# Optimization experiments

Measured on AMD Instinct MI355X. Metric: run time of the kernel, lower is better.

The kernel has to match this reference:

```python
import jax, jax.numpy as jnp
import numpy as np

RADIUS = 2                 # soft detection radius (init kwarg)
NMS_RADIUS = 2             # hardcoded in detect_keypoints: simple_nms(scores, 2)
TOP_K = 4096
TEMPERATURE = 0.1
KSIZE = 2 * RADIUS + 1     # 5
KK = KSIZE * KSIZE         # 25


def _hw_grid(dtype):
    # flatten order j = dy*KSIZE + dx ; entry = (x_off, y_off)  (torch's [:, [1,0]])
    lin = jnp.linspace(-RADIUS, RADIUS, KSIZE, dtype=dtype)
    gx, gy = jnp.meshgrid(lin, lin)  # 'xy': gx[dy,dx]=lin[dx], gy[dy,dx]=lin[dy]
    return jnp.stack([gx, gy], axis=-1).reshape(-1, 2)  # (KK, 2)


def _maxpool(x, r):
    k = 2 * r + 1
    return jax.lax.reduce_window(x, -jnp.inf, jax.lax.max,
                                 (1, 1, k, k), (1, 1, 1, 1),
                                 ((0, 0), (0, 0), (r, r), (r, r)))


def _simple_nms(scores, r):
    zeros = jnp.zeros_like(scores)
    max_mask = scores == _maxpool(scores, r)
    for _ in range(2):
        supp_mask = _maxpool(max_mask.astype(scores.dtype), r) > 0
        supp_scores = jnp.where(supp_mask, zeros, scores)
        new_max_mask = supp_scores == _maxpool(supp_scores, r)
        max_mask = max_mask | (new_max_mask & ~supp_mask)
    return jnp.where(max_mask, scores, zeros)


def _bilinear_zeros(img, xy):
    # img: (h, w); xy: (K, 2) normalized [-1,1]; align_corners=True, zero padding
    h, w = img.shape
    px = (xy[:, 0] + 1.0) * 0.5 * (w - 1)
    py = (xy[:, 1] + 1.0) * 0.5 * (h - 1)
    x0 = jnp.floor(px); y0 = jnp.floor(py)
    wx1 = px - x0; wx0 = 1.0 - wx1
    wy1 = py - y0; wy0 = 1.0 - wy1
    def tap(xi, yi, wgt):
        valid = (xi >= 0) & (xi < w) & (yi >= 0) & (yi < h)
        xc = jnp.clip(xi, 0, w - 1).astype(jnp.int32)
        yc = jnp.clip(yi, 0, h - 1).astype(jnp.int32)
        return jnp.where(valid, img[yc, xc], 0.0) * wgt
    return (tap(x0, y0, wx0 * wy0) + tap(x0 + 1, y0, wx1 * wy0)
            + tap(x0, y0 + 1, wx0 * wy1) + tap(x0 + 1, y0 + 1, wx1 * wy1))


def _dkd_forward(scores_map):
    b, c, h, w = scores_map.shape
    dtype = scores_map.dtype
    scores_nograd = jax.lax.stop_gradient(scores_map)

    nms_scores = _simple_nms(scores_nograd, NMS_RADIUS)
    # zero out border band of width RADIUS
    ybad = (jnp.arange(h) < RADIUS) | (jnp.arange(h) >= h - RADIUS)
    xbad = (jnp.arange(w) < RADIUS) | (jnp.arange(w) >= w - RADIUS)
    border = ybad[:, None] | xbad[None, :]
    nms_scores = jnp.where(border[None, None], 0.0, nms_scores)

    # top-k over flattened score map (per image)
    _, idx = jax.lax.top_k(nms_scores.reshape(b, -1), TOP_K)  # (b, K)
    ix = idx % w
    iy = idx // w

    # patch gather == unfold(scores_map) + gather, done sparsely with zero pad
    padded = jnp.pad(scores_map[:, 0], ((0, 0), (RADIUS, RADIUS), (RADIUS, RADIUS)))
    off = jnp.arange(KSIZE)
    ys = iy[:, :, None] + off[None, None, :]           # (b, K, KSIZE)
    xs = ix[:, :, None] + off[None, None, :]
    bidx = jnp.arange(b)[:, None, None, None]
    patch_scores = padded[bidx, ys[:, :, :, None], xs[:, :, None, :]]  # (b,K,KSIZE,KSIZE)
    patch_scores = patch_scores.reshape(b, TOP_K, KK)

    hw_grid = _hw_grid(dtype)                          # (KK, 2)
    max_v = jax.lax.stop_gradient(patch_scores.max(axis=-1, keepdims=True))
    x_exp = jnp.exp((patch_scores - max_v) / TEMPERATURE)   # (b,K,KK)
    x_exp_sum = x_exp.sum(axis=-1, keepdims=True)            # (b,K,1)
    xy_residual = jnp.einsum('bkp,pd->bkd', x_exp, hw_grid) / x_exp_sum  # (b,K,2)
    hw_dist2 = (((hw_grid[None, None] - xy_residual[:, :, None]) / RADIUS) ** 2).sum(-1)
    scoredispersity = (x_exp * hw_dist2).sum(-1) / x_exp_sum[..., 0]     # (b,K)

    keypoints_xy_nms = jnp.stack([ix, iy], axis=-1).astype(dtype)
    wh = jnp.array([w - 1, h - 1], dtype=dtype)
    keypoints_xy = (keypoints_xy_nms + xy_residual) / wh * 2.0 - 1.0     # (b,K,2)

    kptscore = jax.vmap(_bilinear_zeros)(scores_map[:, 0], keypoints_xy)  # (b,K)
    return keypoints_xy, kptscore, scoredispersity


def setup_inputs() -> dict:
    key = jax.random.key(0)
    scores_map = jax.random.uniform(key, (8, 1, 1024, 1024), dtype=jnp.float32)
    return {"scores_map": scores_map}


def reference(scores_map):
    # matches torch forward: (keypoints, kptscores, scoredispersitys)
    return _dkd_forward(scores_map)
```

## Files before the change

kernel.cpp:

```cpp
#include <hip/hip_runtime.h>
#include <stdint.h>

namespace {

constexpr int B = 8;
constexpr int H = 1024;
constexpr int W = 1024;
constexpr int TOPK = 4096;
constexpr int CAND_CAP = 131072;
constexpr int SEL_CAP = 16384;
constexpr int LIST_CAP = 320;
constexpr int HIST_N = 32768;
constexpr int NCHUNK = 32;
constexpr int NHB = 48;

constexpr int RROWS = 92;
constexpr int NG = 22;
constexpr int STR = 88;
constexpr int MW4 = 4;
constexpr int NSTRIP = 11;
constexpr int NUNIT = NG * NSTRIP;

constexpr int RK_ME = 256;
constexpr int RK_CH = 1024;

constexpr size_t OFF_CNT   = 0;
constexpr size_t OFF_GHIST = 4096;
constexpr size_t OFF_RANK  = OFF_GHIST + (size_t)B * HIST_N * 4;
constexpr size_t OFF_SEL   = OFF_RANK + (size_t)B * SEL_CAP * 4;
constexpr size_t OFF_TOPK  = OFF_SEL + (size_t)B * SEL_CAP * 8;
constexpr size_t OFF_CAND  = OFF_TOPK + (size_t)B * TOPK * 8;
constexpr size_t MEMSET_BYTES = OFF_RANK + (size_t)B * SEL_CAP * 4;

__device__ __forceinline__ float max5(float a, float b, float c, float d, float e) {
  return fmaxf(fmaxf(fmaxf(a, b), fmaxf(c, d)), e);
}
__device__ __forceinline__ float4 ld4(const float* p) {
  return *reinterpret_cast<const float4*>(p);
}

template <int PASS>
__device__ __forceinline__ void score_pass(
    int u, int x0, int y0, const float* __restrict__ S,
    const uint32_t* __restrict__ SUP, uint32_t* __restrict__ MA,
    uint64_t* list, uint32_t* cnt_loc, uint64_t* cand, uint32_t* cand_count, int b) {
  const int G = u % NG, s = u / NG;
  const int r0 = 2 + 8 * s;
  const int gx0 = x0 - 12 + 4 * G;
  uint32_t colm = 0;
#pragma unroll
  for (int j = 0; j < 4; ++j)
    if ((unsigned)(gx0 + j) < (unsigned)W) colm |= 1u << j;
  const int p = 4 * G - 4;
  const int pw = (p < 0) ? 0 : (p >> 5);
  const int psh = (p < 0) ? 0 : (p & 31);
  const int pls = (p < 0) ? -p : 0;

  float4 hw[5], cw[5];
  uint32_t sn[5];
#pragma unroll
  for (int k = 0; k < 12; ++k) {
    const int rr = r0 - 2 + k;
    const float* rowp = S + rr * STR + 4 * G;
    float4 d = ld4(rowp);
    float4 a = (G > 0) ? ld4(rowp - 4) : d;
    float4 e = (G < NG - 1) ? ld4(rowp + 4) : d;
    uint32_t supn = 0;
    if (PASS != 0) {
      const uint32_t* srow = SUP + rr * MW4;
      uint64_t X = (uint64_t)srow[pw] | ((uint64_t)srow[pw + 1] << 32);
      uint64_t win = pls ? (X << pls) : (X >> psh);
      if (win & 0x001u) a.x = 0.f;
      if (win & 0x002u) a.y = 0.f;
      if (win & 0x004u) a.z = 0.f;
      if (win & 0x008u) a.w = 0.f;
      if (win & 0x010u) d.x = 0.f;
      if (win & 0x020u) d.y = 0.f;
      if (win & 0x040u) d.z = 0.f;
      if (win & 0x080u) d.w = 0.f;
      if (win & 0x100u) e.x = 0.f;
      if (win & 0x200u) e.y = 0.f;
      if (win & 0x400u) e.z = 0.f;
      if (win & 0x800u) e.w = 0.f;
      supn = (uint32_t)(win >> 4) & 0xFu;
    }
    float4 hm;
    hm.x = max5(a.z, a.w, d.x, d.y, d.z);
    hm.y = max5(a.w, d.x, d.y, d.z, d.w);
    hm.z = max5(d.x, d.y, d.z, d.w, e.x);
    hm.w = max5(d.y, d.z, d.w, e.x, e.y);
    hw[k % 5] = hm;
    cw[k % 5] = d;
    sn[k % 5] = supn;
    if (k >= 4) {
      const int rq = r0 + k - 4;
      const int gy = y0 - 12 + rq;
      float4 vm;
      vm.x = max5(hw[0].x, hw[1].x, hw[2].x, hw[3].x, hw[4].x);
      vm.y = max5(hw[0].y, hw[1].y, hw[2].y, hw[3].y, hw[4].y);
      vm.z = max5(hw[0].z, hw[1].z, hw[2].z, hw[3].z, hw[4].z);
      vm.w = max5(hw[0].w, hw[1].w, hw[2].w, hw[3].w, hw[4].w);
      float4 c = cw[(k + 3) % 5];
      uint32_t nm = (uint32_t)(c.x == vm.x) | ((uint32_t)(c.y == vm.y) << 1) |
                    ((uint32_t)(c.z == vm.z) << 2) | ((uint32_t)(c.w == vm.w) << 3);
      nm &= ((unsigned)gy < (unsigned)H) ? colm : 0u;
      const int widx = rq * MW4 + (G >> 3);
      const int shift = 4 * (G & 7);
      if (PASS == 0) {
        if (nm) atomicOr(&MA[widx], nm << shift);
      } else if (PASS == 1) {
        uint32_t v = nm & ~sn[(k + 3) % 5];
        if (v) atomicOr(&MA[widx], v << shift);
      } else {
        uint32_t fin = ((MA[widx] >> shift) & 0xFu) | (nm & ~sn[(k + 3) % 5]);
        if (fin && G >= 3 && G < 19 && rq >= 12 && rq < 76 && gy >= 2 && gy < H - 2) {
#pragma unroll
          for (int j = 0; j < 4; ++j) {
            if ((fin >> j) & 1u) {
              int gx = gx0 + j;
              if (gx >= 2 && gx < W - 2) {
                float sval = S[rq * STR + 4 * G + j];
                if (sval > 0.0f) {
                  uint32_t bits = __float_as_uint(sval);
                  uint32_t flat = (uint32_t)(gy * W + gx);
                  uint64_t key = ((uint64_t)bits << 32) | (uint64_t)(0xFFFFFFFFu - flat);
                  uint32_t pos = atomicAdd(cnt_loc, 1u);
                  if (pos < (uint32_t)LIST_CAP) {
                    list[pos] = key;
                  } else {
                    uint32_t pp = atomicAdd(&cand_count[b], 1u);
                    if (pp < (uint32_t)CAND_CAP) cand[(size_t)b * CAND_CAP + pp] = key;
                  }
                }
              }
            }
          }
        }
      }
    }
  }
}

__device__ __forceinline__ void dilate_pass(int u, int x0, int y0,
                                            const uint32_t* __restrict__ MIN_,
                                            uint32_t* __restrict__ SOUT) {
  const int G = u % NG, s = u / NG;
  const int r0 = 2 + 8 * s;
  const int gx0 = x0 - 12 + 4 * G;
  uint32_t colm = 0;
#pragma unroll
  for (int j = 0; j < 4; ++j)
    if ((unsigned)(gx0 + j) < (unsigned)W) colm |= 1u << j;
  const int p = 4 * G - 2;
  const int pw = (p < 0) ? 0 : (p >> 5);
  const int psh = (p < 0) ? 0 : (p & 31);
  const int pls = (p < 0) ? -p : 0;
  uint32_t ring[5];
#pragma unroll
  for (int k = 0; k < 12; ++k) {
    const int rr = r0 - 2 + k;
    const uint32_t* srow = MIN_ + rr * MW4;
    uint64_t X = (uint64_t)srow[pw] | ((uint64_t)srow[pw + 1] << 32);
    uint64_t win = pls ? (X << pls) : (X >> psh);
    uint64_t t = win | (win >> 1) | (win >> 2) | (win >> 3) | (win >> 4);
    ring[k % 5] = (uint32_t)t & 0xFu;
    if (k >= 4) {
      const int rq = r0 + k - 4;
      const int gy = y0 - 12 + rq;
      uint32_t nib = ring[0] | ring[1] | ring[2] | ring[3] | ring[4];
      nib &= ((unsigned)gy < (unsigned)H) ? colm : 0u;
      if (nib) atomicOr(&SOUT[rq * MW4 + (G >> 3)], nib << (4 * (G & 7)));
    }
  }
}

__global__ void __launch_bounds__(256, 4) k_nms(const float* __restrict__ scores,
                                                uint64_t* __restrict__ cand,
                                                uint32_t* __restrict__ cand_count) {
  __shared__ float S[RROWS * STR];
  __shared__ uint32_t MAs[RROWS * MW4];
  __shared__ uint32_t SP1[RROWS * MW4];
  __shared__ uint32_t SP2[RROWS * MW4];
  __shared__ uint64_t list[LIST_CAP];
  __shared__ uint32_t cnt_loc, base_g;
  const int b = blockIdx.z;
  const int x0 = blockIdx.x * 64, y0 = blockIdx.y * 64;
  const int tid = threadIdx.x;
  const float* img = scores + (size_t)b * H * W;
  if (tid == 0) cnt_loc = 0;

  for (int u = tid; u < RROWS * NG; u += 256) {
    int r = u / NG, G = u % NG;
    int gy = y0 - 12 + r, gx = x0 - 12 + 4 * G;
    float4 v;
    if ((unsigned)gy < (unsigned)H && (unsigned)gx < (unsigned)W)
      v = ld4(img + (size_t)gy * W + gx);
    else
      v = make_float4(-INFINITY, -INFINITY, -INFINITY, -INFINITY);
    *reinterpret_cast<float4*>(&S[r * STR + 4 * G]) = v;
  }
  for (int i = tid; i < RROWS * MW4; i += 256) {
    MAs[i] = 0;
    SP1[i] = 0;
    SP2[i] = 0;
  }
  __syncthreads();
  if (tid < NUNIT)
    score_pass<0>(tid, x0, y0, S, nullptr, MAs, nullptr, nullptr, nullptr, nullptr, b);
  __syncthreads();
  if (tid < NUNIT) dilate_pass(tid, x0, y0, MAs, SP1);
  __syncthreads();
  if (tid < NUNIT)
    score_pass<1>(tid, x0, y0, S, SP1, MAs, nullptr, nullptr, nullptr, nullptr, b);
  __syncthreads();
  if (tid < NUNIT) dilate_pass(tid, x0, y0, MAs, SP2);
  __syncthreads();
  if (tid < NUNIT)
    score_pass<2>(tid, x0, y0, S, SP2, MAs, list, &cnt_loc, cand, cand_count, b);
  __syncthreads();
  uint32_t nblk = cnt_loc;
  uint32_t nmain = nblk < (uint32_t)LIST_CAP ? nblk : (uint32_t)LIST_CAP;
  if (tid == 0) base_g = atomicAdd(&cand_count[b], nmain);
  __syncthreads();
  uint32_t bg = base_g;
  for (uint32_t i = tid; i < nmain; i += 256) {
    uint32_t pp = bg + i;
    if (pp < (uint32_t)CAND_CAP) cand[(size_t)b * CAND_CAP + pp] = list[i];
  }
}

__global__ void __launch_bounds__(256) k_hist(const uint64_t* __restrict__ cand,
                                              const uint32_t* __restrict__ cand_count,
                                              uint32_t* __restrict__ ghist) {
  const int b = blockIdx.y;
  uint32_t n = cand_count[b];
  if (n > (uint32_t)CAND_CAP) n = CAND_CAP;
  uint32_t* gh = ghist + (size_t)b * HIST_N;
  const uint64_t* cb = cand + (size_t)b * CAND_CAP;
  const int lane = threadIdx.x & 63;
  for (uint32_t i = blockIdx.x * 256 + threadIdx.x;; i += NHB * 256) {
    bool valid = i < n;
    uint64_t act = __ballot(valid);
    if (!act) break;
    uint32_t bkt = 0;
    if (valid) bkt = (uint32_t)(cb[i] >> 47);
    uint64_t peers = act;
#pragma unroll
    for (int bit = 0; bit < 15; ++bit) {
      uint64_t bb = __ballot((bkt >> bit) & 1u);
      peers &= ((bkt >> bit) & 1u) ? bb : ~bb;
    }
    if (valid && (__ffsll((unsigned long long)peers) - 1) == lane)
      atomicAdd(&gh[bkt], (uint32_t)__popcll((unsigned long long)peers));
  }
}

__global__ void __launch_bounds__(256) k_chunksum(const uint32_t* __restrict__ ghist,
                                                  uint32_t* __restrict__ gchunk) {
  const int b = blockIdx.y, c = blockIdx.x;
  const uint32_t* gh = ghist + (size_t)b * HIST_N + c * 1024;
  uint32_t s = 0;
#pragma unroll
  for (int j = 0; j < 4; ++j) s += gh[threadIdx.x + 256 * j];
#pragma unroll
  for (int m = 1; m < 64; m <<= 1) s += __shfl_xor(s, m);
  __shared__ uint32_t red[4];
  if ((threadIdx.x & 63) == 0) red[threadIdx.x >> 6] = s;
  __syncthreads();
  if (threadIdx.x == 0) gchunk[b * NCHUNK + c] = red[0] + red[1] + red[2] + red[3];
}

__global__ void __launch_bounds__(1024) k_findthr(const uint32_t* __restrict__ ghist,
                                                  const uint32_t* __restrict__ gchunk,
                                                  uint64_t* __restrict__ thr_key) {
  __shared__ uint32_t ch[NCHUNK];
  __shared__ uint32_t h[1024];
  __shared__ int shCC;
  __shared__ uint32_t sh_above;
  const int b = blockIdx.x, t = threadIdx.x;
  if (t < NCHUNK) ch[t] = gchunk[b * NCHUNK + t];
  __syncthreads();
  if (t == 0) {
    uint32_t run = 0;
    int CC = -1;
    uint32_t above = 0;
    for (int c = NCHUNK - 1; c >= 0; --c) {
      uint32_t nrun = run + ch[c];
      if (run < (uint32_t)TOPK && nrun >= (uint32_t)TOPK) { CC = c; above = run; }
      run = nrun;
    }
    if (run < (uint32_t)TOPK) CC = -1;
    shCC = CC;
    sh_above = above;
  }
  __syncthreads();
  const int CC = shCC;
  if (CC < 0) {
    if (t == 0) thr_key[b] = 0ull;
    return;
  }
  const uint32_t above = sh_above;
  h[t] = ghist[(size_t)b * HIST_N + CC * 1024 + t];
  __syncthreads();
  for (int d = 1; d < 1024; d <<= 1) {
    uint32_t v = (t + d < 1024) ? h[t + d] : 0u;
    __syncthreads();
    h[t] += v;
    __syncthreads();
  }
  uint32_t cum = above + h[t];
  uint32_t cumn = (t + 1 < 1024) ? above + h[t + 1] : above;
  if (cum >= (uint32_t)TOPK && cumn < (uint32_t)TOPK)
    thr_key[b] = (uint64_t)(CC * 1024 + t) << 47;
}

__global__ void __launch_bounds__(1024) k_compact(const uint64_t* __restrict__ cand,
                                                  const uint32_t* __restrict__ cand_count,
                                                  const uint64_t* __restrict__ thr_key,
                                                  uint64_t* __restrict__ sel,
                                                  uint32_t* __restrict__ sel_count) {
  __shared__ uint64_t list[1024];
  __shared__ uint32_t cnt_loc;
  __shared__ uint32_t base_g;
  const int b = blockIdx.y;
  uint32_t n = cand_count[b];
  if (n > (uint32_t)CAND_CAP) n = CAND_CAP;
  const int tid = threadIdx.x;
  if (tid == 0) cnt_loc = 0;
  __syncthreads();
  uint32_t i = blockIdx.x * 1024 + tid;
  if (i < n) {
    uint64_t key = cand[(size_t)b * CAND_CAP + i];
    if (key >= thr_key[b]) {
      uint32_t pos = atomicAdd(&cnt_loc, 1u);
      list[pos] = key;
    }
  }
  __syncthreads();
  uint32_t nblk = cnt_loc;
  if (tid == 0 && nblk > 0) base_g = atomicAdd(&sel_count[b], nblk);
  __syncthreads();
  if (nblk > 0 && (uint32_t)tid < nblk) {
    uint32_t pp = base_g + tid;
    if (pp < (uint32_t)SEL_CAP) sel[(size_t)b * SEL_CAP + pp] = list[tid];
  }
}

__global__ void __launch_bounds__(RK_ME) k_rank_part(const uint64_t* __restrict__ sel,
                                                     const uint32_t* __restrict__ sel_count,
                                                     uint32_t* __restrict__ rankg) {
  __shared__ uint64_t keys[RK_CH];
  const int b = blockIdx.z;
  uint32_t n = sel_count[b];
  if (n > (uint32_t)SEL_CAP) n = SEL_CAP;
  const uint32_t me0 = blockIdx.x * RK_ME;
  const uint32_t c0 = blockIdx.y * RK_CH;
  if (me0 >= n || c0 >= n) return;
  const uint64_t* sb = sel + (size_t)b * SEL_CAP;
  uint32_t clen = n - c0;
  if (clen > (uint32_t)RK_CH) clen = RK_CH;
  for (uint32_t i = threadIdx.x; i < clen; i += RK_ME) keys[i] = sb[c0 + i];
  __syncthreads();
  const uint32_t me = me0 + threadIdx.x;
  if (me >= n) return;
  const uint64_t kme = sb[me];
  uint32_t rank = 0;
  uint32_t i = 0;
  for (; i + 8 <= clen; i += 8) {
    rank += (keys[i] > kme);
    rank += (keys[i + 1] > kme);
    rank += (keys[i + 2] > kme);
    rank += (keys[i + 3] > kme);
    rank += (keys[i + 4] > kme);
    rank += (keys[i + 5] > kme);
    rank += (keys[i + 6] > kme);
    rank += (keys[i + 7] > kme);
  }
  for (; i < clen; ++i) rank += (keys[i] > kme);
  if (rank) atomicAdd(&rankg[(size_t)b * SEL_CAP + me], rank);
}

__global__ void __launch_bounds__(256) k_scatter(const uint64_t* __restrict__ sel,
                                                 const uint32_t* __restrict__ sel_count,
                                                 const uint32_t* __restrict__ rankg,
                                                 uint64_t* __restrict__ topk) {
  const int b = blockIdx.y;
  uint32_t n = sel_count[b];
  if (n > (uint32_t)SEL_CAP) n = SEL_CAP;
  uint32_t i = blockIdx.x * 256 + threadIdx.x;
  if (i >= n) return;
  uint32_t r = rankg[(size_t)b * SEL_CAP + i];
  if (r < (uint32_t)TOPK) topk[(size_t)b * TOPK + r] = sel[(size_t)b * SEL_CAP + i];
}

__global__ void __launch_bounds__(256) k_refine(const float* __restrict__ scores,
                                                const uint64_t* __restrict__ topk,
                                                float* __restrict__ out) {
  int gid = blockIdx.x * 256 + threadIdx.x;
  int kp = gid >> 3, ln = gid & 7;
  const int b = kp / TOPK;
  const int k = kp % TOPK;
  uint64_t key = topk[(size_t)b * TOPK + k];
  uint32_t flat = 0xFFFFFFFFu - (uint32_t)(key & 0xFFFFFFFFull);
  if (flat >= (uint32_t)(H * W)) flat = 0;
  const int ix = (int)(flat % W);
  const int iy = (int)(flat / W);
  const float* img = scores + (size_t)b * H * W;

  const int nt = (ln == 0) ? 4 : 3;
  float v[4];
  float mymax = -INFINITY;
#pragma unroll
  for (int i = 0; i < 4; ++i) {
    if (i < nt) {
      int t = ln + 8 * i;
      int y = iy + t / 5 - 2, x = ix + t % 5 - 2;
      float val = ((unsigned)x < (unsigned)W && (unsigned)y < (unsigned)H)
                      ? img[(size_t)y * W + x] : 0.0f;
      v[i] = val;
      mymax = fmaxf(mymax, val);
    }
  }
#pragma unroll
  for (int m = 1; m < 8; m <<= 1) mymax = fmaxf(mymax, __shfl_xor(mymax, m));
  float e[4];
  float sum = 0.f, sx = 0.f, sy = 0.f;
#pragma unroll
  for (int i = 0; i < 4; ++i) {
    if (i < nt) {
      int t = ln + 8 * i;
      float ev = expf((v[i] - mymax) / 0.1f);
      e[i] = ev;
      sum += ev;
      sx += ev * (float)(t % 5 - 2);
      sy += ev * (float)(t / 5 - 2);
    }
  }
#pragma unroll
  for (int m = 1; m < 8; m <<= 1) {
    sum += __shfl_xor(sum, m);
    sx += __shfl_xor(sx, m);
    sy += __shfl_xor(sy, m);
  }
  float rx = sx / sum, ry = sy / sum;
  float dsp = 0.f;
#pragma unroll
  for (int i = 0; i < 4; ++i) {
    if (i < nt) {
      int t = ln + 8 * i;
      float dx = ((float)(t % 5 - 2) - rx) * 0.5f;
      float dy = ((float)(t / 5 - 2) - ry) * 0.5f;
      dsp += e[i] * (dx * dx + dy * dy);
    }
  }
#pragma unroll
  for (int m = 1; m < 8; m <<= 1) dsp += __shfl_xor(dsp, m);
  if (ln != 0) return;
  dsp /= sum;
  float kx = ((float)ix + rx) / 1023.0f * 2.0f - 1.0f;
  float ky = ((float)iy + ry) / 1023.0f * 2.0f - 1.0f;
  float px = (kx + 1.0f) * 0.5f * 1023.0f;
  float py = (ky + 1.0f) * 0.5f * 1023.0f;
  float x0f = floorf(px), y0f = floorf(py);
  float wx1 = px - x0f, wx0 = 1.0f - wx1;
  float wy1 = py - y0f, wy0 = 1.0f - wy1;
  int x0 = (int)x0f, y0 = (int)y0f;
  float sc = 0.0f;
  {
    int xs[2] = {x0, x0 + 1};
    int ys[2] = {y0, y0 + 1};
    float wxs[2] = {wx0, wx1};
    float wys[2] = {wy0, wy1};
#pragma unroll
    for (int yy = 0; yy < 2; ++yy)
#pragma unroll
      for (int xx = 0; xx < 2; ++xx) {
        int xi = xs[xx], yi = ys[yy];
        bool valid = (xi >= 0 && xi < W && yi >= 0 && yi < H);
        int xc = min(max(xi, 0), W - 1);
        int yc = min(max(yi, 0), H - 1);
        float vv = valid ? img[(size_t)yc * W + xc] : 0.0f;
        sc += vv * (wxs[xx] * wys[yy]);
      }
  }
  out[((size_t)b * TOPK + k) * 2 + 0] = kx;
  out[((size_t)b * TOPK + k) * 2 + 1] = ky;
  out[(size_t)B * TOPK * 2 + (size_t)b * TOPK + k] = sc;
  out[(size_t)B * TOPK * 3 + (size_t)b * TOPK + k] = dsp;
}

}

extern "C" void kernel_launch(void* const* d_in, const int* in_sizes, int n_in,
                              void* d_out, int out_size, void* d_ws, size_t ws_size,
                              hipStream_t stream) {
  const float* scores = (const float*)d_in[0];
  float* out = (float*)d_out;
  char* ws = (char*)d_ws;

  uint32_t* cnt = (uint32_t*)(ws + OFF_CNT);
  uint32_t* cand_count = cnt;
  uint32_t* sel_count  = cnt + 8;
  uint64_t* thr_key    = (uint64_t*)(cnt + 16);
  uint32_t* gchunk     = cnt + 256;
  uint32_t* ghist = (uint32_t*)(ws + OFF_GHIST);
  uint32_t* rankg = (uint32_t*)(ws + OFF_RANK);
  uint64_t* sel  = (uint64_t*)(ws + OFF_SEL);
  uint64_t* topk = (uint64_t*)(ws + OFF_TOPK);
  uint64_t* cand = (uint64_t*)(ws + OFF_CAND);

  hipMemsetAsync(ws + OFF_CNT, 0, MEMSET_BYTES, stream);

  k_nms<<<dim3(W / 64, H / 64, B), 256, 0, stream>>>(scores, cand, cand_count);
  k_hist<<<dim3(NHB, B), 256, 0, stream>>>(cand, cand_count, ghist);
  k_chunksum<<<dim3(NCHUNK, B), 256, 0, stream>>>(ghist, gchunk);
  k_findthr<<<B, 1024, 0, stream>>>(ghist, gchunk, thr_key);
  k_compact<<<dim3(CAND_CAP / 1024, B), 1024, 0, stream>>>(cand, cand_count, thr_key, sel, sel_count);
  k_rank_part<<<dim3(SEL_CAP / RK_ME, SEL_CAP / RK_CH, B), RK_ME, 0, stream>>>(sel, sel_count, rankg);
  k_scatter<<<dim3(SEL_CAP / 256, B), 256, 0, stream>>>(sel, sel_count, rankg, topk);
  k_refine<<<(B * TOPK * 8) / 256, 256, 0, stream>>>(scores, topk, out);
}
```

Baseline: 224.9 us.

## Fuse rank, scatter and refine kernels; merge chunk-sum into threshold search

The rank-partial, scatter and refine kernels become one kernel. Each block ranks its slice of selected keys against all selected keys in shared-memory chunks, then refines the keypoints and writes them straight to their rank position. Chunk summation is folded into the threshold kernel, which now builds a 1024-way coarse prefix scan followed by a serial fine search. The memset is replaced with a zeroing kernel, and the selection capacity is halved. These changes remove several launches and the global rank and topk buffers, but each rank block now loops over every key serially, and a halved SEL_CAP could overflow if ties at the threshold bucket are large.

Result: slower. 269.1 us (+19.6%).

```diff
diff --git a/kernel.cpp b/kernel.cpp
--- a/kernel.cpp
+++ b/kernel.cpp
@@ -8,10 +8,9 @@
 constexpr int W = 1024;
 constexpr int TOPK = 4096;
 constexpr int CAND_CAP = 131072;
-constexpr int SEL_CAP = 16384;
+constexpr int SEL_CAP = 8192;
 constexpr int LIST_CAP = 320;
 constexpr int HIST_N = 32768;
-constexpr int NCHUNK = 32;
 constexpr int NHB = 48;
 
 constexpr int RROWS = 92;
@@ -21,16 +20,13 @@
 constexpr int NSTRIP = 11;
 constexpr int NUNIT = NG * NSTRIP;
 
-constexpr int RK_ME = 256;
 constexpr int RK_CH = 1024;
 
 constexpr size_t OFF_CNT   = 0;
 constexpr size_t OFF_GHIST = 4096;
-constexpr size_t OFF_RANK  = OFF_GHIST + (size_t)B * HIST_N * 4;
-constexpr size_t OFF_SEL   = OFF_RANK + (size_t)B * SEL_CAP * 4;
-constexpr size_t OFF_TOPK  = OFF_SEL + (size_t)B * SEL_CAP * 8;
-constexpr size_t OFF_CAND  = OFF_TOPK + (size_t)B * TOPK * 8;
-constexpr size_t MEMSET_BYTES = OFF_RANK + (size_t)B * SEL_CAP * 4;
+constexpr size_t OFF_SEL   = OFF_GHIST + (size_t)B * HIST_N * 4;
+constexpr size_t OFF_CAND  = OFF_SEL + (size_t)B * SEL_CAP * 8;
+constexpr size_t ZERO_BYTES = OFF_SEL;
 
 __device__ __forceinline__ float max5(float a, float b, float c, float d, float e) {
   return fmaxf(fmaxf(fmaxf(a, b), fmaxf(c, d)), e);
@@ -229,6 +225,13 @@
   }
 }
 
+__global__ void __launch_bounds__(256) k_zero(float4* __restrict__ p, int n4) {
+  int i = blockIdx.x * 256 + threadIdx.x;
+  const int stride = gridDim.x * 256;
+  const float4 z = make_float4(0.f, 0.f, 0.f, 0.f);
+  for (; i < n4; i += stride) p[i] = z;
+}
+
 __global__ void __launch_bounds__(256) k_hist(const uint64_t* __restrict__ cand,
                                               const uint32_t* __restrict__ cand_count,
                                               uint32_t* __restrict__ ghist) {
@@ -255,63 +258,45 @@
   }
 }
 
-__global__ void __launch_bounds__(256) k_chunksum(const uint32_t* __restrict__ ghist,
-                                                  uint32_t* __restrict__ gchunk) {
-  const int b = blockIdx.y, c = blockIdx.x;
-  const uint32_t* gh = ghist + (size_t)b * HIST_N + c * 1024;
-  uint32_t s = 0;
-#pragma unroll
-  for (int j = 0; j < 4; ++j) s += gh[threadIdx.x + 256 * j];
-#pragma unroll
-  for (int m = 1; m < 64; m <<= 1) s += __shfl_xor(s, m);
-  __shared__ uint32_t red[4];
-  if ((threadIdx.x & 63) == 0) red[threadIdx.x >> 6] = s;
-  __syncthreads();
-  if (threadIdx.x == 0) gchunk[b * NCHUNK + c] = red[0] + red[1] + red[2] + red[3];
-}
-
 __global__ void __launch_bounds__(1024) k_findthr(const uint32_t* __restrict__ ghist,
-                                                  const uint32_t* __restrict__ gchunk,
                                                   uint64_t* __restrict__ thr_key) {
-  __shared__ uint32_t ch[NCHUNK];
-  __shared__ uint32_t h[1024];
-  __shared__ int shCC;
+  __shared__ uint32_t part[1024];
+  __shared__ int shT;
   __shared__ uint32_t sh_above;
   const int b = blockIdx.x, t = threadIdx.x;
-  if (t < NCHUNK) ch[t] = gchunk[b * NCHUNK + t];
-  __syncthreads();
-  if (t == 0) {
-    uint32_t run = 0;
-    int CC = -1;
-    uint32_t above = 0;
-    for (int c = NCHUNK - 1; c >= 0; --c) {
-      uint32_t nrun = run + ch[c];
-      if (run < (uint32_t)TOPK && nrun >= (uint32_t)TOPK) { CC = c; above = run; }
-      run = nrun;
-    }
-    if (run < (uint32_t)TOPK) CC = -1;
-    shCC = CC;
-    sh_above = above;
-  }
-  __syncthreads();
-  const int CC = shCC;
-  if (CC < 0) {
+  const uint32_t* gh = ghist + (size_t)b * HIST_N;
+  uint32_t s = 0;
+#pragma unroll 4
+  for (int i = 0; i < 32; ++i) s += gh[t * 32 + i];
+  part[t] = s;
+  if (t == 0) { shT = -1; sh_above = 0; }
+  __syncthreads();
+  for (int d = 1; d < 1024; d <<= 1) {
+    uint32_t v = (t + d < 1024) ? part[t + d] : 0u;
+    __syncthreads();
+    part[t] += v;
+    __syncthreads();
+  }
+  if (part[0] < (uint32_t)TOPK) {
     if (t == 0) thr_key[b] = 0ull;
     return;
   }
-  const uint32_t above = sh_above;
-  h[t] = ghist[(size_t)b * HIST_N + CC * 1024 + t];
-  __syncthreads();
-  for (int d = 1; d < 1024; d <<= 1) {
-    uint32_t v = (t + d < 1024) ? h[t + d] : 0u;
-    __syncthreads();
-    h[t] += v;
-    __syncthreads();
-  }
-  uint32_t cum = above + h[t];
-  uint32_t cumn = (t + 1 < 1024) ? above + h[t + 1] : above;
-  if (cum >= (uint32_t)TOPK && cumn < (uint32_t)TOPK)
-    thr_key[b] = (uint64_t)(CC * 1024 + t) << 47;
+  {
+    uint32_t mine = part[t];
+    uint32_t nxt = (t + 1 < 1024) ? part[t + 1] : 0u;
+    if (mine >= (uint32_t)TOPK && nxt < (uint32_t)TOPK) { shT = t; sh_above = nxt; }
+  }
+  __syncthreads();
+  if (t == 0) {
+    const int T = shT;
+    uint32_t run = sh_above;
+    int bkt = T * 32;
+    for (int i = 31; i >= 0; --i) {
+      run += gh[T * 32 + i];
+      if (run >= (uint32_t)TOPK) { bkt = T * 32 + i; break; }
+    }
+    thr_key[b] = (uint64_t)bkt << 47;
+  }
 }
 
 __global__ void __launch_bounds__(1024) k_compact(const uint64_t* __restrict__ cand,
@@ -346,147 +331,139 @@
   }
 }
 
-__global__ void __launch_bounds__(RK_ME) k_rank_part(const uint64_t* __restrict__ sel,
-                                                     const uint32_t* __restrict__ sel_count,
-                                                     uint32_t* __restrict__ rankg) {
+__global__ void __launch_bounds__(256) k_rankref(const float* __restrict__ scores,
+                                                 const uint64_t* __restrict__ sel,
+                                                 const uint32_t* __restrict__ sel_count,
+                                                 float* __restrict__ out) {
   __shared__ uint64_t keys[RK_CH];
-  const int b = blockIdx.z;
-  uint32_t n = sel_count[b];
-  if (n > (uint32_t)SEL_CAP) n = SEL_CAP;
-  const uint32_t me0 = blockIdx.x * RK_ME;
-  const uint32_t c0 = blockIdx.y * RK_CH;
-  if (me0 >= n || c0 >= n) return;
-  const uint64_t* sb = sel + (size_t)b * SEL_CAP;
-  uint32_t clen = n - c0;
-  if (clen > (uint32_t)RK_CH) clen = RK_CH;
-  for (uint32_t i = threadIdx.x; i < clen; i += RK_ME) keys[i] = sb[c0 + i];
-  __syncthreads();
-  const uint32_t me = me0 + threadIdx.x;
-  if (me >= n) return;
-  const uint64_t kme = sb[me];
-  uint32_t rank = 0;
-  uint32_t i = 0;
-  for (; i + 8 <= clen; i += 8) {
-    rank += (keys[i] > kme);
-    rank += (keys[i + 1] > kme);
-    rank += (keys[i + 2] > kme);
-    rank += (keys[i + 3] > kme);
-    rank += (keys[i + 4] > kme);
-    rank += (keys[i + 5] > kme);
-    rank += (keys[i + 6] > kme);
-    rank += (keys[i + 7] > kme);
-  }
-  for (; i < clen; ++i) rank += (keys[i] > kme);
-  if (rank) atomicAdd(&rankg[(size_t)b * SEL_CAP + me], rank);
-}
-
-__global__ void __launch_bounds__(256) k_scatter(const uint64_t* __restrict__ sel,
-                                                 const uint32_t* __restrict__ sel_count,
-                                                 const uint32_t* __restrict__ rankg,
-                                                 uint64_t* __restrict__ topk) {
+  __shared__ uint64_t kks[256];
+  __shared__ uint32_t rks[256];
   const int b = blockIdx.y;
   uint32_t n = sel_count[b];
   if (n > (uint32_t)SEL_CAP) n = SEL_CAP;
-  uint32_t i = blockIdx.x * 256 + threadIdx.x;
-  if (i >= n) return;
-  uint32_t r = rankg[(size_t)b * SEL_CAP + i];
-  if (r < (uint32_t)TOPK) topk[(size_t)b * TOPK + r] = sel[(size_t)b * SEL_CAP + i];
-}
-
-__global__ void __launch_bounds__(256) k_refine(const float* __restrict__ scores,
-                                                const uint64_t* __restrict__ topk,
-                                                float* __restrict__ out) {
-  int gid = blockIdx.x * 256 + threadIdx.x;
-  int kp = gid >> 3, ln = gid & 7;
-  const int b = kp / TOPK;
-  const int k = kp % TOPK;
-  uint64_t key = topk[(size_t)b * TOPK + k];
-  uint32_t flat = 0xFFFFFFFFu - (uint32_t)(key & 0xFFFFFFFFull);
-  if (flat >= (uint32_t)(H * W)) flat = 0;
-  const int ix = (int)(flat % W);
-  const int iy = (int)(flat / W);
+  const uint32_t me0 = blockIdx.x * 256;
+  if (me0 >= n) return;
+  const uint64_t* sb = sel + (size_t)b * SEL_CAP;
+  const int tid = threadIdx.x;
+  const uint32_t me = me0 + tid;
+  const uint64_t kme = (me < n) ? sb[me] : 0ull;
+  uint32_t rank = 0;
+  for (uint32_t c0 = 0; c0 < n; c0 += RK_CH) {
+    uint32_t clen = n - c0;
+    if (clen > (uint32_t)RK_CH) clen = RK_CH;
+    __syncthreads();
+    for (uint32_t i = tid; i < clen; i += 256) keys[i] = sb[c0 + i];
+    __syncthreads();
+    uint32_t i = 0;
+    for (; i + 8 <= clen; i += 8) {
+      rank += (keys[i] > kme);
+      rank += (keys[i + 1] > kme);
+      rank += (keys[i + 2] > kme);
+      rank += (keys[i + 3] > kme);
+      rank += (keys[i + 4] > kme);
+      rank += (keys[i + 5] > kme);
+      rank += (keys[i + 6] > kme);
+      rank += (keys[i + 7] > kme);
+    }
+    for (; i < clen; ++i) rank += (keys[i] > kme);
+  }
+  rks[tid] = (me < n && rank < (uint32_t)TOPK) ? rank : 0xFFFFFFFFu;
+  kks[tid] = kme;
+  __syncthreads();
+
   const float* img = scores + (size_t)b * H * W;
-
-  const int nt = (ln == 0) ? 4 : 3;
-  float v[4];
-  float mymax = -INFINITY;
-#pragma unroll
-  for (int i = 0; i < 4; ++i) {
-    if (i < nt) {
-      int t = ln + 8 * i;
-      int y = iy + t / 5 - 2, x = ix + t % 5 - 2;
-      float val = ((unsigned)x < (unsigned)W && (unsigned)y < (unsigned)H)
-                      ? img[(size_t)y * W + x] : 0.0f;
-      v[i] = val;
-      mymax = fmaxf(mymax, val);
-    }
-  }
-#pragma unroll
-  for (int m = 1; m < 8; m <<= 1) mymax = fmaxf(mymax, __shfl_xor(mymax, m));
-  float e[4];
-  float sum = 0.f, sx = 0.f, sy = 0.f;
-#pragma unroll
-  for (int i = 0; i < 4; ++i) {
-    if (i < nt) {
-      int t = ln + 8 * i;
-      float ev = expf((v[i] - mymax) / 0.1f);
-      e[i] = ev;
-      sum += ev;
-      sx += ev * (float)(t % 5 - 2);
-      sy += ev * (float)(t / 5 - 2);
-    }
-  }
-#pragma unroll
-  for (int m = 1; m < 8; m <<= 1) {
-    sum += __shfl_xor(sum, m);
-    sx += __shfl_xor(sx, m);
-    sy += __shfl_xor(sy, m);
-  }
-  float rx = sx / sum, ry = sy / sum;
-  float dsp = 0.f;
-#pragma unroll
-  for (int i = 0; i < 4; ++i) {
-    if (i < nt) {
-      int t = ln + 8 * i;
-      float dx = ((float)(t % 5 - 2) - rx) * 0.5f;
-      float dy = ((float)(t / 5 - 2) - ry) * 0.5f;
-      dsp += e[i] * (dx * dx + dy * dy);
-    }
-  }
-#pragma unroll
-  for (int m = 1; m < 8; m <<= 1) dsp += __shfl_xor(dsp, m);
-  if (ln != 0) return;
-  dsp /= sum;
-  float kx = ((float)ix + rx) / 1023.0f * 2.0f - 1.0f;
-  float ky = ((float)iy + ry) / 1023.0f * 2.0f - 1.0f;
-  float px = (kx + 1.0f) * 0.5f * 1023.0f;
-  float py = (ky + 1.0f) * 0.5f * 1023.0f;
-  float x0f = floorf(px), y0f = floorf(py);
-  float wx1 = px - x0f, wx0 = 1.0f - wx1;
-  float wy1 = py - y0f, wy0 = 1.0f - wy1;
-  int x0 = (int)x0f, y0 = (int)y0f;
-  float sc = 0.0f;
-  {
-    int xs[2] = {x0, x0 + 1};
-    int ys[2] = {y0, y0 + 1};
-    float wxs[2] = {wx0, wx1};
-    float wys[2] = {wy0, wy1};
-#pragma unroll
-    for (int yy = 0; yy < 2; ++yy)
-#pragma unroll
-      for (int xx = 0; xx < 2; ++xx) {
-        int xi = xs[xx], yi = ys[yy];
-        bool valid = (xi >= 0 && xi < W && yi >= 0 && yi < H);
-        int xc = min(max(xi, 0), W - 1);
-        int yc = min(max(yi, 0), H - 1);
-        float vv = valid ? img[(size_t)yc * W + xc] : 0.0f;
-        sc += vv * (wxs[xx] * wys[yy]);
+  const int ln = tid & 7;
+#pragma unroll 1
+  for (int round = 0; round < 8; ++round) {
+    const int ki = (tid >> 3) + 32 * round;
+    const uint32_t r = rks[ki];
+    if (r == 0xFFFFFFFFu) continue;
+    uint64_t key = kks[ki];
+    uint32_t flat = 0xFFFFFFFFu - (uint32_t)(key & 0xFFFFFFFFull);
+    const int ix = (int)(flat % W);
+    const int iy = (int)(flat / W);
+
+    const int nt = (ln == 0) ? 4 : 3;
+    float v[4];
+    float mymax = -INFINITY;
+#pragma unroll
+    for (int i = 0; i < 4; ++i) {
+      if (i < nt) {
+        int t = ln + 8 * i;
+        int y = iy + t / 5 - 2, x = ix + t % 5 - 2;
+        float val = ((unsigned)x < (unsigned)W && (unsigned)y < (unsigned)H)
+                        ? img[(size_t)y * W + x] : 0.0f;
+        v[i] = val;
+        mymax = fmaxf(mymax, val);
       }
-  }
-  out[((size_t)b * TOPK + k) * 2 + 0] = kx;
-  out[((size_t)b * TOPK + k) * 2 + 1] = ky;
-  out[(size_t)B * TOPK * 2 + (size_t)b * TOPK + k] = sc;
-  out[(size_t)B * TOPK * 3 + (size_t)b * TOPK + k] = dsp;
+    }
+#pragma unroll
+    for (int m = 1; m < 8; m <<= 1) mymax = fmaxf(mymax, __shfl_xor(mymax, m));
+    float e[4];
+    float sum = 0.f, sx = 0.f, sy = 0.f;
+#pragma unroll
+    for (int i = 0; i < 4; ++i) {
+      if (i < nt) {
+        int t = ln + 8 * i;
+        float ev = expf((v[i] - mymax) / 0.1f);
+        e[i] = ev;
+        sum += ev;
+        sx += ev * (float)(t % 5 - 2);
+        sy += ev * (float)(t / 5 - 2);
+      }
+    }
+#pragma unroll
+    for (int m = 1; m < 8; m <<= 1) {
+      sum += __shfl_xor(sum, m);
+      sx += __shfl_xor(sx, m);
+      sy += __shfl_xor(sy, m);
+    }
+    float rx = sx / sum, ry = sy / sum;
+    float dsp = 0.f;
+#pragma unroll
+    for (int i = 0; i < 4; ++i) {
+      if (i < nt) {
+        int t = ln + 8 * i;
+        float dx = ((float)(t % 5 - 2) - rx) * 0.5f;
+        float dy = ((float)(t / 5 - 2) - ry) * 0.5f;
+        dsp += e[i] * (dx * dx + dy * dy);
+      }
+    }
+#pragma unroll
+    for (int m = 1; m < 8; m <<= 1) dsp += __shfl_xor(dsp, m);
+    if (ln != 0) continue;
+    dsp /= sum;
+    float kx = ((float)ix + rx) / 1023.0f * 2.0f - 1.0f;
+    float ky = ((float)iy + ry) / 1023.0f * 2.0f - 1.0f;
+    float px = (kx + 1.0f) * 0.5f * 1023.0f;
+    float py = (ky + 1.0f) * 0.5f * 1023.0f;
+    float x0f = floorf(px), y0f = floorf(py);
+    float wx1 = px - x0f, wx0 = 1.0f - wx1;
+    float wy1 = py - y0f, wy0 = 1.0f - wy1;
+    int x0 = (int)x0f, y0 = (int)y0f;
+    float sc = 0.0f;
+    {
+      int xs[2] = {x0, x0 + 1};
+      int ys[2] = {y0, y0 + 1};
+      float wxs[2] = {wx0, wx1};
+      float wys[2] = {wy0, wy1};
+#pragma unroll
+      for (int yy = 0; yy < 2; ++yy)
+#pragma unroll
+        for (int xx = 0; xx < 2; ++xx) {
+          int xi = xs[xx], yi = ys[yy];
+          bool valid = (xi >= 0 && xi < W && yi >= 0 && yi < H);
+          int xc = min(max(xi, 0), W - 1);
+          int yc = min(max(yi, 0), H - 1);
+          float vv = valid ? img[(size_t)yc * W + xc] : 0.0f;
+          sc += vv * (wxs[xx] * wys[yy]);
+        }
+    }
+    out[((size_t)b * TOPK + r) * 2 + 0] = kx;
+    out[((size_t)b * TOPK + r) * 2 + 1] = ky;
+    out[(size_t)B * TOPK * 2 + (size_t)b * TOPK + r] = sc;
+    out[(size_t)B * TOPK * 3 + (size_t)b * TOPK + r] = dsp;
+  }
 }
 
 }
@@ -502,21 +479,14 @@
   uint32_t* cand_count = cnt;
   uint32_t* sel_count  = cnt + 8;
   uint64_t* thr_key    = (uint64_t*)(cnt + 16);
-  uint32_t* gchunk     = cnt + 256;
   uint32_t* ghist = (uint32_t*)(ws + OFF_GHIST);
-  uint32_t* rankg = (uint32_t*)(ws + OFF_RANK);
   uint64_t* sel  = (uint64_t*)(ws + OFF_SEL);
-  uint64_t* topk = (uint64_t*)(ws + OFF_TOPK);
   uint64_t* cand = (uint64_t*)(ws + OFF_CAND);
 
-  hipMemsetAsync(ws + OFF_CNT, 0, MEMSET_BYTES, stream);
-
+  k_zero<<<256, 256, 0, stream>>>((float4*)ws, (int)(ZERO_BYTES / 16));
   k_nms<<<dim3(W / 64, H / 64, B), 256, 0, stream>>>(scores, cand, cand_count);
   k_hist<<<dim3(NHB, B), 256, 0, stream>>>(cand, cand_count, ghist);
-  k_chunksum<<<dim3(NCHUNK, B), 256, 0, stream>>>(ghist, gchunk);
-  k_findthr<<<B, 1024, 0, stream>>>(ghist, gchunk, thr_key);
+  k_findthr<<<B, 1024, 0, stream>>>(ghist, thr_key);
   k_compact<<<dim3(CAND_CAP / 1024, B), 1024, 0, stream>>>(cand, cand_count, thr_key, sel, sel_count);
-  k_rank_part<<<dim3(SEL_CAP / RK_ME, SEL_CAP / RK_CH, B), RK_ME, 0, stream>>>(sel, sel_count, rankg);
-  k_scatter<<<dim3(SEL_CAP / 256, B), 256, 0, stream>>>(sel, sel_count, rankg, topk);
-  k_refine<<<(B * TOPK * 8) / 256, 256, 0, stream>>>(scores, topk, out);
-}
+  k_rankref<<<dim3(SEL_CAP / 256, B), 256, 0, stream>>>(scores, sel, sel_count, out);
+}
```
